# Performance work log

Measured on AMD Instinct MI355X. Metric: run time of the kernel, lower is better.

The kernel has to match this reference:

```python
import jax, jax.numpy as jnp
import numpy as np

B, A = 65536, 32          # batch, n_agents
D, H1, H2, L = 4, 32, 32, 16  # local MLP dims
G_IN, G_H, G_OUT = 2 * L, 32, 2  # global MLP dims


def _lin_init(k, fan_in, fan_out):
    kw, kb = jax.random.split(k)
    s = 1.0 / np.sqrt(fan_in)
    W = jax.random.uniform(kw, (fan_in, fan_out), minval=-s, maxval=s, dtype=jnp.float32)
    b = jax.random.uniform(kb, (fan_out,), minval=-s, maxval=s, dtype=jnp.float32)
    return W, b


def setup_inputs() -> dict:
    key = jax.random.key(0)
    ks = jax.random.split(key, 9)
    x = jax.random.uniform(ks[0], (B, A * D), dtype=jnp.float32)
    oW1, ob1 = _lin_init(ks[1], D, H1)
    oW2, ob2 = _lin_init(ks[2], H1, H2)
    oW3, ob3 = _lin_init(ks[3], H2, L)
    sW1, sb1 = _lin_init(ks[4], D, H1)
    sW2, sb2 = _lin_init(ks[5], H1, H2)
    sW3, sb3 = _lin_init(ks[6], H2, L)
    gW1, gb1 = _lin_init(ks[7], G_IN, G_H)
    gW2, gb2 = _lin_init(ks[8], G_H, G_OUT)
    return {
        "joint_state_actions": x,
        "selected_agent_idx": 5,
        "oW1": oW1, "ob1": ob1, "oW2": oW2, "ob2": ob2, "oW3": oW3, "ob3": ob3,
        "sW1": sW1, "sb1": sb1, "sW2": sW2, "sb2": sb2, "sW3": sW3, "sb3": sb3,
        "gW1": gW1, "gb1": gb1, "gW2": gW2, "gb2": gb2,
    }


def _mlp3(x, W1, b1, W2, b2, W3, b3):
    h = jax.nn.relu(x @ W1 + b1)
    h = jax.nn.relu(h @ W2 + b2)
    return jax.nn.relu(h @ W3 + b3)


def reference(joint_state_actions, selected_agent_idx,
              oW1, ob1, oW2, ob2, oW3, ob3,
              sW1, sb1, sW2, sb2, sW3, sb3,
              gW1, gb1, gW2, gb2):
    xa = joint_state_actions.reshape(-1, A, D)  # [B, A, 4]
    # other-agents stack applied to all agents at once, masked sum over non-selected
    other = _mlp3(xa, oW1, ob1, oW2, ob2, oW3, ob3)  # [B, A, 16]
    mask = (jnp.arange(A) != selected_agent_idx).astype(other.dtype)[None, :, None]
    sum_other = jnp.sum(other * mask, axis=1)  # [B, 16]
    sel_in = xa[:, selected_agent_idx]  # [B, 4] (static index)
    sel_out = _mlp3(sel_in, sW1, sb1, sW2, sb2, sW3, sb3)  # [B, 16]
    h = jax.nn.relu(jnp.concatenate([sel_out, sum_other], axis=1) @ gW1 + gb1)
    q = h @ gW2 + gb2  # [B, 2]
    actions = sel_in[:, 3].astype(jnp.int32)[:, None]  # [B, 1]
    return jnp.take_along_axis(q, actions, axis=1)  # [B, 1]
```

## Files before the change

### kernel.cpp

```cpp
#include <hip/hip_runtime.h>
#include <hip/hip_bf16.h>

#define DEV __device__ __forceinline__

typedef __attribute__((ext_vector_type(8)))  __bf16    bf16x8;
typedef __attribute__((ext_vector_type(4)))  int       int4v;
typedef __attribute__((ext_vector_type(2)))  unsigned  uint2v;
typedef __attribute__((ext_vector_type(16))) float     vfloat16;

#if __has_builtin(__builtin_amdgcn_permlane32_swap)
#define HAVE_PLSWAP 1
#endif

DEV int pkbf(float a, float b) {
    __hip_bfloat162 h = __float22bfloat162_rn(make_float2(a, b));
    int r;
    __builtin_memcpy(&r, &h, sizeof(r));
    return r;
}

DEV bf16x8 i4_to_frag(int4v v) { return __builtin_bit_cast(bf16x8, v); }

DEV vfloat16 mfma32(bf16x8 a, bf16x8 b, vfloat16 c) {
    return __builtin_amdgcn_mfma_f32_32x32x16_bf16(a, b, c, 0, 0, 0);
}

DEV bf16x8 xposeB(float c0, float c1, float c2, float c3,
                  float c4, float c5, float c6, float c7, bool h) {
    int R0 = pkbf(fmaxf(c0, 0.f), fmaxf(c1, 0.f));
    int R1 = pkbf(fmaxf(c2, 0.f), fmaxf(c3, 0.f));
    int R2 = pkbf(fmaxf(c4, 0.f), fmaxf(c5, 0.f));
    int R3 = pkbf(fmaxf(c6, 0.f), fmaxf(c7, 0.f));
#ifdef HAVE_PLSWAP
    uint2v p0 = __builtin_amdgcn_permlane32_swap((unsigned)R0, (unsigned)R2, false, false);
    uint2v p1 = __builtin_amdgcn_permlane32_swap((unsigned)R1, (unsigned)R3, false, false);
    int4v v;
    v.x = (int)p0.x; v.y = (int)p1.x; v.z = (int)p0.y; v.w = (int)p1.y;
#else
    int S0 = h ? R0 : R2;
    int S1 = h ? R1 : R3;
    int Y0 = __shfl_xor(S0, 32, 64);
    int Y1 = __shfl_xor(S1, 32, 64);
    int4v v;
    v.x = h ? Y0 : R0;
    v.y = h ? Y1 : R1;
    v.z = h ? R2 : Y0;
    v.w = h ? R3 : Y1;
#endif
    return i4_to_frag(v);
}

DEV bf16x8 make_afrag(const float* __restrict__ W, int ld, int Mact, int K,
                      int koff, int lane) {
    int m = lane & 31;
    int h = lane >> 5;
    int d[4];
#pragma unroll
    for (int i = 0; i < 4; ++i) {
        int k0 = koff + h * 8 + 2 * i;
        int k1 = k0 + 1;
        float w0 = 0.f, w1 = 0.f;
        if (m < Mact) {
            if (k0 < K) w0 = W[k0 * ld + m];
            if (k1 < K) w1 = W[k1 * ld + m];
        }
        d[i] = pkbf(w0, w1);
    }
    int4v v; v.x = d[0]; v.y = d[1]; v.z = d[2]; v.w = d[3];
    return i4_to_frag(v);
}

DEV vfloat16 bvec32(const float* __restrict__ b, int lane) {
    int h = lane >> 5;
    vfloat16 v;
#pragma unroll
    for (int reg = 0; reg < 16; ++reg)
        v[reg] = b[(reg & 3) + 8 * (reg >> 2) + 4 * h];
    return v;
}
DEV vfloat16 bvec16(const float* __restrict__ b, int lane) {
    int h = lane >> 5;
    vfloat16 v;
#pragma unroll
    for (int reg = 0; reg < 16; ++reg)
        v[reg] = (reg < 8) ? b[(reg & 3) + 8 * (reg >> 2) + 4 * h] : 0.f;
    return v;
}

DEV bf16x8 make_b1(float4 xa) {
    int4v v;
    v.x = pkbf(xa.x, xa.y);
    v.y = pkbf(xa.z, xa.w);
    v.z = 0;
    v.w = 0;
    return i4_to_frag(v);
}

struct Frags {
    bf16x8 A1, A2lo, A2hi, A3lo, A3hi;
    vfloat16 c1, b2, b3;
};

DEV void load_frags(Frags& F,
                    const float* __restrict__ W1, const float* __restrict__ b1,
                    const float* __restrict__ W2, const float* __restrict__ b2,
                    const float* __restrict__ W3, const float* __restrict__ b3,
                    int lane) {
    F.A1   = make_afrag(W1, 32, 32, 4, 0, lane);
    F.A2lo = make_afrag(W2, 32, 32, 32, 0, lane);
    F.A2hi = make_afrag(W2, 32, 32, 32, 16, lane);
    F.A3lo = make_afrag(W3, 16, 16, 32, 0, lane);
    F.A3hi = make_afrag(W3, 16, 16, 32, 16, lane);
    F.c1 = bvec32(b1, lane);
    F.b2 = bvec32(b2, lane);
    F.b3 = bvec16(b3, lane);
}

DEV vfloat16 run_mlp3(bf16x8 B1, const Frags& F, bool h) {
    vfloat16 C = mfma32(F.A1, B1, F.c1);
    bf16x8 Blo = xposeB(C[0], C[1], C[2], C[3], C[4], C[5], C[6], C[7], h);
    bf16x8 Bhi = xposeB(C[8], C[9], C[10], C[11], C[12], C[13], C[14], C[15], h);
    vfloat16 C2 = mfma32(F.A2lo, Blo, F.b2);
    C2 = mfma32(F.A2hi, Bhi, C2);
    Blo = xposeB(C2[0], C2[1], C2[2], C2[3], C2[4], C2[5], C2[6], C2[7], h);
    Bhi = xposeB(C2[8], C2[9], C2[10], C2[11], C2[12], C2[13], C2[14], C2[15], h);
    vfloat16 C3 = mfma32(F.A3lo, Blo, F.b3);
    C3 = mfma32(F.A3hi, Bhi, C3);
    return C3;
}

__global__ __launch_bounds__(256, 3)
void dqn_kernel(const float* __restrict__ x, const int* __restrict__ selp,
                const float* __restrict__ oW1, const float* __restrict__ ob1,
                const float* __restrict__ oW2, const float* __restrict__ ob2,
                const float* __restrict__ oW3, const float* __restrict__ ob3,
                const float* __restrict__ sW1, const float* __restrict__ sb1,
                const float* __restrict__ sW2, const float* __restrict__ sb2,
                const float* __restrict__ sW3, const float* __restrict__ sb3,
                const float* __restrict__ gW1, const float* __restrict__ gb1,
                const float* __restrict__ gW2, const float* __restrict__ gb2,
                float* __restrict__ out)
{
    __shared__ float lds[2][8][64];

    const int tid  = threadIdx.x;
    const int lane = tid & 63;
    const int wave = tid >> 6;
    const int pair = wave >> 1;
    const bool oddw = (wave & 1) != 0;
    const bool h = lane >= 32;
    const int c = lane & 31;
    const int sel = *selp;
    const int base = (blockIdx.x * 2 + pair) * 32;

    Frags Fo;
    load_frags(Fo, oW1, ob1, oW2, ob2, oW3, ob3, lane);

    const float* xrow = x + (size_t)(base + c) * 128;

    float sum[8] = {0.f, 0.f, 0.f, 0.f, 0.f, 0.f, 0.f, 0.f};
    const int a0 = oddw ? 16 : 0;

    float4 xa = make_float4(0.f, 0.f, 0.f, 0.f);
    if (!h) xa = *(const float4*)(xrow + 4 * a0);
#pragma unroll 2
    for (int a = a0; a < a0 + 16; ++a) {
        float4 xn = make_float4(0.f, 0.f, 0.f, 0.f);
        if (!h && (a + 1 < a0 + 16)) xn = *(const float4*)(xrow + 4 * (a + 1));
        bf16x8 B1 = make_b1(xa);
        vfloat16 C3 = run_mlp3(B1, Fo, h);
        if (a != sel) {
#pragma unroll
            for (int i = 0; i < 8; ++i) sum[i] += fmaxf(C3[i], 0.f);
        }
        xa = xn;
    }

    if (oddw) {
#pragma unroll
        for (int i = 0; i < 8; ++i) lds[pair][i][lane] = sum[i];
    }
    __syncthreads();
    if (!oddw) {
#pragma unroll
        for (int i = 0; i < 8; ++i) sum[i] += lds[pair][i][lane];

        Frags Fs;
        load_frags(Fs, sW1, sb1, sW2, sb2, sW3, sb3, lane);

        float4 xs = make_float4(0.f, 0.f, 0.f, 0.f);
        if (!h) xs = *(const float4*)(xrow + 4 * sel);
        vfloat16 C3s = run_mlp3(make_b1(xs), Fs, h);

        bf16x8 Ag_lo = make_afrag(gW1, 32, 32, 32, 0, lane);
        bf16x8 Ag_hi = make_afrag(gW1, 32, 32, 32, 16, lane);
        vfloat16 gb1v = bvec32(gb1, lane);
        bf16x8 Bg_lo = xposeB(C3s[0], C3s[1], C3s[2], C3s[3],
                              C3s[4], C3s[5], C3s[6], C3s[7], h);
        bf16x8 Bg_hi = xposeB(sum[0], sum[1], sum[2], sum[3],
                              sum[4], sum[5], sum[6], sum[7], h);
        vfloat16 G = mfma32(Ag_lo, Bg_lo, gb1v);
        G = mfma32(Ag_hi, Bg_hi, G);
#pragma unroll
        for (int i = 0; i < 16; ++i) G[i] = fmaxf(G[i], 0.f);

        float q0 = 0.f, q1 = 0.f;
#pragma unroll
        for (int reg = 0; reg < 16; ++reg) {
            int row = (reg & 3) + 8 * (reg >> 2) + (h ? 4 : 0);
            q0 += G[reg] * gW2[row * 2 + 0];
            q1 += G[reg] * gW2[row * 2 + 1];
        }
        q0 += __shfl_xor(q0, 32, 64);
        q1 += __shfl_xor(q1, 32, 64);
        q0 += gb2[0];
        q1 += gb2[1];

        if (!h) {
            int act = (int)xs.w;
            act = act < 0 ? 0 : (act > 1 ? 1 : act);
            out[base + c] = act ? q1 : q0;
        }
    }
}

extern "C" void kernel_launch(void* const* d_in, const int* in_sizes, int n_in,
                              void* d_out, int out_size, void* d_ws, size_t ws_size,
                              hipStream_t stream) {
    const float* x   = (const float*)d_in[0];
    const int*   sel = (const int*)d_in[1];
    const float* oW1 = (const float*)d_in[2];
    const float* ob1 = (const float*)d_in[3];
    const float* oW2 = (const float*)d_in[4];
    const float* ob2 = (const float*)d_in[5];
    const float* oW3 = (const float*)d_in[6];
    const float* ob3 = (const float*)d_in[7];
    const float* sW1 = (const float*)d_in[8];
    const float* sb1 = (const float*)d_in[9];
    const float* sW2 = (const float*)d_in[10];
    const float* sb2 = (const float*)d_in[11];
    const float* sW3 = (const float*)d_in[12];
    const float* sb3 = (const float*)d_in[13];
    const float* gW1 = (const float*)d_in[14];
    const float* gb1 = (const float*)d_in[15];
    const float* gW2 = (const float*)d_in[16];
    const float* gb2 = (const float*)d_in[17];
    float* out = (float*)d_out;

    const int B = in_sizes[0] / 128;
    const int blocks = B / 64;
    dqn_kernel<<<blocks, 256, 0, stream>>>(x, sel,
                                           oW1, ob1, oW2, ob2, oW3, ob3,
                                           sW1, sb1, sW2, sb2, sW3, sb3,
                                           gW1, gb1, gW2, gb2, out);
}
```

Measured before the change: 134.2 us.

## Stage x tile in LDS, split agents across four waves, fold layer-1 bias into MFMA

```diff
diff --git a/kernel.cpp b/kernel.cpp
--- a/kernel.cpp
+++ b/kernel.cpp
@@ -50,8 +50,8 @@
     return i4_to_frag(v);
 }
 
-DEV bf16x8 make_afrag(const float* __restrict__ W, int ld, int Mact, int K,
-                      int koff, int lane) {
+DEV bf16x8 make_afrag(const float* __restrict__ W, const float* __restrict__ bias,
+                      int ld, int Mact, int K, int koff, int lane) {
     int m = lane & 31;
     int h = lane >> 5;
     int d[4];
@@ -62,7 +62,9 @@
         float w0 = 0.f, w1 = 0.f;
         if (m < Mact) {
             if (k0 < K) w0 = W[k0 * ld + m];
+            else if (bias && k0 == K) w0 = bias[m];
             if (k1 < K) w1 = W[k1 * ld + m];
+            else if (bias && k1 == K) w1 = bias[m];
         }
         d[i] = pkbf(w0, w1);
     }
@@ -87,18 +89,25 @@
     return v;
 }
 
-DEV bf16x8 make_b1(float4 xa) {
+DEV vfloat16 zero16() {
+    vfloat16 z;
+#pragma unroll
+    for (int i = 0; i < 16; ++i) z[i] = 0.f;
+    return z;
+}
+
+DEV bf16x8 make_b1h(float4 xa, bool h) {
     int4v v;
-    v.x = pkbf(xa.x, xa.y);
-    v.y = pkbf(xa.z, xa.w);
-    v.z = 0;
+    v.x = h ? 0 : pkbf(xa.x, xa.y);
+    v.y = h ? 0 : pkbf(xa.z, xa.w);
+    v.z = h ? 0 : 0x00003f80;
     v.w = 0;
     return i4_to_frag(v);
 }
 
 struct Frags {
     bf16x8 A1, A2lo, A2hi, A3lo, A3hi;
-    vfloat16 c1, b2, b3;
+    vfloat16 b2, b3;
 };
 
 DEV void load_frags(Frags& F,
@@ -106,18 +115,17 @@
                     const float* __restrict__ W2, const float* __restrict__ b2,
                     const float* __restrict__ W3, const float* __restrict__ b3,
                     int lane) {
-    F.A1   = make_afrag(W1, 32, 32, 4, 0, lane);
-    F.A2lo = make_afrag(W2, 32, 32, 32, 0, lane);
-    F.A2hi = make_afrag(W2, 32, 32, 32, 16, lane);
-    F.A3lo = make_afrag(W3, 16, 16, 32, 0, lane);
-    F.A3hi = make_afrag(W3, 16, 16, 32, 16, lane);
-    F.c1 = bvec32(b1, lane);
+    F.A1   = make_afrag(W1, b1,      32, 32, 4,  0,  lane);
+    F.A2lo = make_afrag(W2, nullptr, 32, 32, 32, 0,  lane);
+    F.A2hi = make_afrag(W2, nullptr, 32, 32, 32, 16, lane);
+    F.A3lo = make_afrag(W3, nullptr, 16, 16, 32, 0,  lane);
+    F.A3hi = make_afrag(W3, nullptr, 16, 16, 32, 16, lane);
     F.b2 = bvec32(b2, lane);
     F.b3 = bvec16(b3, lane);
 }
 
 DEV vfloat16 run_mlp3(bf16x8 B1, const Frags& F, bool h) {
-    vfloat16 C = mfma32(F.A1, B1, F.c1);
+    vfloat16 C = mfma32(F.A1, B1, zero16());
     bf16x8 Blo = xposeB(C[0], C[1], C[2], C[3], C[4], C[5], C[6], C[7], h);
     bf16x8 Bhi = xposeB(C[8], C[9], C[10], C[11], C[12], C[13], C[14], C[15], h);
     vfloat16 C2 = mfma32(F.A2lo, Blo, F.b2);
@@ -129,7 +137,9 @@
     return C3;
 }
 
-__global__ __launch_bounds__(256, 3)
+#define XSTRIDE 132
+
+__global__ __launch_bounds__(256, 4)
 void dqn_kernel(const float* __restrict__ x, const int* __restrict__ selp,
                 const float* __restrict__ oW1, const float* __restrict__ ob1,
                 const float* __restrict__ oW2, const float* __restrict__ ob2,
@@ -141,34 +151,43 @@
                 const float* __restrict__ gW2, const float* __restrict__ gb2,
                 float* __restrict__ out)
 {
-    __shared__ float lds[2][8][64];
+    __shared__ float lds_x[32 * XSTRIDE];
+    __shared__ float lds_red[3][8][64];
 
     const int tid  = threadIdx.x;
     const int lane = tid & 63;
     const int wave = tid >> 6;
-    const int pair = wave >> 1;
-    const bool oddw = (wave & 1) != 0;
     const bool h = lane >= 32;
     const int c = lane & 31;
     const int sel = *selp;
-    const int base = (blockIdx.x * 2 + pair) * 32;
+    const int base0 = blockIdx.x * 32;
+
+    {
+        const float* xblk = x + (size_t)base0 * 128;
+#pragma unroll
+        for (int k = 0; k < 4; ++k) {
+            int f = tid + 256 * k;
+            int row = f >> 5;
+            int ag  = f & 31;
+            float4 v = *(const float4*)(xblk + (size_t)f * 4);
+            *(float4*)&lds_x[ag * XSTRIDE + row * 4] = v;
+        }
+    }
 
     Frags Fo;
     load_frags(Fo, oW1, ob1, oW2, ob2, oW3, ob3, lane);
 
-    const float* xrow = x + (size_t)(base + c) * 128;
+    __syncthreads();
 
     float sum[8] = {0.f, 0.f, 0.f, 0.f, 0.f, 0.f, 0.f, 0.f};
-    const int a0 = oddw ? 16 : 0;
-
-    float4 xa = make_float4(0.f, 0.f, 0.f, 0.f);
-    if (!h) xa = *(const float4*)(xrow + 4 * a0);
-#pragma unroll 2
-    for (int a = a0; a < a0 + 16; ++a) {
-        float4 xn = make_float4(0.f, 0.f, 0.f, 0.f);
-        if (!h && (a + 1 < a0 + 16)) xn = *(const float4*)(xrow + 4 * (a + 1));
-        bf16x8 B1 = make_b1(xa);
-        vfloat16 C3 = run_mlp3(B1, Fo, h);
+    const int a0 = wave * 8;
+
+    float4 xa = *(const float4*)&lds_x[a0 * XSTRIDE + c * 4];
+#pragma unroll
+    for (int a = a0; a < a0 + 8; ++a) {
+        int an = (a + 1 < a0 + 8) ? a + 1 : a;
+        float4 xn = *(const float4*)&lds_x[an * XSTRIDE + c * 4];
+        vfloat16 C3 = run_mlp3(make_b1h(xa, h), Fo, h);
         if (a != sel) {
 #pragma unroll
             for (int i = 0; i < 8; ++i) sum[i] += fmaxf(C3[i], 0.f);
@@ -176,24 +195,25 @@
         xa = xn;
     }
 
-    if (oddw) {
-#pragma unroll
-        for (int i = 0; i < 8; ++i) lds[pair][i][lane] = sum[i];
+    if (wave != 0) {
+#pragma unroll
+        for (int i = 0; i < 8; ++i) lds_red[wave - 1][i][lane] = sum[i];
     }
     __syncthreads();
-    if (!oddw) {
-#pragma unroll
-        for (int i = 0; i < 8; ++i) sum[i] += lds[pair][i][lane];
+
+    if (wave == 0) {
+#pragma unroll
+        for (int j = 0; j < 3; ++j)
+#pragma unroll
+            for (int i = 0; i < 8; ++i) sum[i] += lds_red[j][i][lane];
 
         Frags Fs;
         load_frags(Fs, sW1, sb1, sW2, sb2, sW3, sb3, lane);
-
-        float4 xs = make_float4(0.f, 0.f, 0.f, 0.f);
-        if (!h) xs = *(const float4*)(xrow + 4 * sel);
-        vfloat16 C3s = run_mlp3(make_b1(xs), Fs, h);
-
-        bf16x8 Ag_lo = make_afrag(gW1, 32, 32, 32, 0, lane);
-        bf16x8 Ag_hi = make_afrag(gW1, 32, 32, 32, 16, lane);
+        float4 xs = *(const float4*)&lds_x[sel * XSTRIDE + c * 4];
+        vfloat16 C3s = run_mlp3(make_b1h(xs, h), Fs, h);
+
+        bf16x8 Ag_lo = make_afrag(gW1, nullptr, 32, 32, 32, 0,  lane);
+        bf16x8 Ag_hi = make_afrag(gW1, nullptr, 32, 32, 32, 16, lane);
         vfloat16 gb1v = bvec32(gb1, lane);
         bf16x8 Bg_lo = xposeB(C3s[0], C3s[1], C3s[2], C3s[3],
                               C3s[4], C3s[5], C3s[6], C3s[7], h);
@@ -219,7 +239,7 @@
         if (!h) {
             int act = (int)xs.w;
             act = act < 0 ? 0 : (act > 1 ? 1 : act);
-            out[base + c] = act ? q1 : q0;
+            out[base0 + c] = act ? q1 : q0;
         }
     }
 }
@@ -248,7 +268,7 @@
     float* out = (float*)d_out;
 
     const int B = in_sizes[0] / 128;
-    const int blocks = B / 64;
+    const int blocks = B / 32;
     dqn_kernel<<<blocks, 256, 0, stream>>>(x, sel,
                                            oW1, ob1, oW2, ob2, oW3, ob3,
                                            sW1, sb1, sW2, sb2, sW3, sb3,
```

Measured after the change: 136.9 us. No clear change (+2.0%).
